# Kernel tuning notes

Hardware: AMD Instinct MI355X
Metric: run time of the kernel (lower is better)

## Reference

```python
import jax, jax.numpy as jnp
import numpy as np

N_SRC = 50000; N_DST = 50000; E = 800000
IN_NODE = 128; IN_EDGE = 16; OUT_NODE = 64; OUT_EDGE = 16; H = 4
LEAKY_SLOPE = 0.01  # F.leaky_relu default used inside dgl EGATConv


def setup_inputs() -> dict:
    key = jax.random.key(0)
    ks = jax.random.split(key, 11)
    return dict(
        nfeats=jax.random.normal(ks[0], (N_SRC, IN_NODE), jnp.float32),
        dst_feats=jax.random.normal(ks[1], (N_DST, IN_NODE), jnp.float32),
        reward=jax.random.uniform(ks[2], (E,), jnp.float32),
        src=jax.random.randint(ks[3], (E,), 0, N_SRC),
        dst=jax.random.randint(ks[4], (E,), 0, N_DST),
        W_ns=jax.random.normal(ks[5], (IN_NODE, H * OUT_NODE), jnp.float32) * 0.05,
        b_ns=jnp.zeros((H * OUT_NODE,), jnp.float32),
        W_ni=jax.random.normal(ks[6], (IN_NODE, H * OUT_EDGE), jnp.float32) * 0.05,
        W_nj=jax.random.normal(ks[7], (IN_NODE, H * OUT_EDGE), jnp.float32) * 0.05,
        W_fij=jax.random.normal(ks[8], (IN_EDGE, H * OUT_EDGE), jnp.float32) * 0.05,
        attn=jax.random.normal(ks[9], (H, OUT_EDGE), jnp.float32) * 0.05,
        b_e=jnp.zeros((H * OUT_EDGE,), jnp.float32),
    )


def reference(nfeats, dst_feats, reward, src, dst,
              W_ns, b_ns, W_ni, W_nj, W_fij, attn, b_e):
    # EGAT.forward with num_layers=1: efeats = reward repeated to IN_EDGE cols
    efeats = jnp.repeat(reward[:, None], IN_EDGE, axis=1)              # (E, Fe_in)
    # --- EGATConv ---
    f_ni = nfeats @ W_ni                                               # (Ns, H*Fe)
    f_nj = dst_feats @ W_nj                                            # (Nd, H*Fe)
    f_out = f_ni[src] + f_nj[dst] + efeats @ W_fij + b_e               # (E, H*Fe)
    f_out = jax.nn.leaky_relu(f_out, LEAKY_SLOPE).reshape(E, H, OUT_EDGE)
    e = jnp.einsum('ehf,hf->eh', f_out, attn)                          # (E, H)
    # edge softmax over incoming edges of each dst node (stable)
    m = jax.ops.segment_max(e, dst, num_segments=N_DST)                # (Nd, H)
    a = jnp.exp(e - m[dst])
    s = jax.ops.segment_sum(a, dst, num_segments=N_DST)                # (Nd, H)
    a = a / jnp.where(s > 0, s, 1.0)[dst]                              # (E, H)
    # weighted aggregation of projected src features
    h_src = (nfeats @ W_ns + b_ns).reshape(N_SRC, H, OUT_NODE)
    msg = h_src[src] * a[:, :, None]                                   # (E, H, Fn)
    h_out = jax.ops.segment_sum(msg, dst, num_segments=N_DST)          # (Nd, H, Fn)
    # wrapper: mean over heads then ReLU
    return jax.nn.relu(h_out.mean(axis=1))                             # (Nd, Fn)
```

## Files before the change

### kernel.cpp

```cpp
#include <hip/hip_runtime.h>

#define IN_NODE 128
#define OUT_NODE 64
#define NHEAD 4
#define HN 256
#define HE 64
#define LEAKY 0.01f

typedef __attribute__((ext_vector_type(8))) short bf16x8;
typedef __attribute__((ext_vector_type(4))) float f32x4;
typedef __attribute__((ext_vector_type(2))) float f32x2;

__device__ __forceinline__ float bf2f(unsigned short u) {
    union { unsigned u; float f; } v; v.u = ((unsigned)u) << 16; return v.f;
}
__device__ __forceinline__ unsigned short f2bf(float x) {
    union { float f; unsigned u; } v; v.f = x;
    unsigned r = v.u + 0x7FFF + ((v.u >> 16) & 1);
    return (unsigned short)(r >> 16);
}
__device__ __forceinline__ bf16x8 cvt8(float4 a, float4 b) {
    bf16x8 r;
    r[0] = (short)f2bf(a.x); r[1] = (short)f2bf(a.y);
    r[2] = (short)f2bf(a.z); r[3] = (short)f2bf(a.w);
    r[4] = (short)f2bf(b.x); r[5] = (short)f2bf(b.y);
    r[6] = (short)f2bf(b.z); r[7] = (short)f2bf(b.w);
    return r;
}
__device__ __forceinline__ f32x2 bfcvt2(unsigned d) {
    union { unsigned u; float f; } lo, hi;
    lo.u = d << 16; hi.u = d & 0xFFFF0000u;
    f32x2 r; r.x = lo.f; r.y = hi.f; return r;
}

__global__ void prep_hist(const float* __restrict__ W_fij,
                          const float* __restrict__ W_ni,
                          const float* __restrict__ W_ns,
                          const float* __restrict__ W_nj,
                          const int* __restrict__ dst,
                          float* __restrict__ wsum, unsigned short* __restrict__ WT,
                          int* __restrict__ cnt, int* __restrict__ rank, int E) {
    int b = blockIdx.x;
    if (b == 0) {
        int k = threadIdx.x;
        if (k < 64) {
            float s = 0.f;
#pragma unroll
            for (int c = 0; c < 16; ++c) s += W_fij[c * 64 + k];
            wsum[k] = s;
        }
        return;
    }
    if (b <= 12) {
        int base = (b - 1) * 4096 + threadIdx.x;
#pragma unroll
        for (int i = 0; i < 16; ++i) {
            int idx = base + i * 256;
            int g   = idx >> 11;
            int rem = idx & 2047;
            int c   = rem >> 9;
            int l   = (rem >> 3) & 63;
            int j   = rem & 7;
            int nl  = l & 15;
            int k   = c * 32 + (l >> 4) * 8 + j;
            unsigned short v;
            if (g < 4)       v = f2bf(W_ni[k * 64  + g * 16 + nl]);
            else if (g < 20) v = f2bf(W_ns[k * 256 + (g - 4) * 16 + nl]);
            else             v = f2bf(W_nj[k * 64  + (g - 20) * 16 + nl]);
            WT[idx] = v;
        }
        return;
    }
    int i = (b - 13) * 256 + threadIdx.x;
    if (i < E) rank[i] = atomicAdd(&cnt[dst[i]], 1);
}

__global__ __launch_bounds__(256) void scan_all(const int* __restrict__ cnt,
                                                int* __restrict__ row_ptr,
                                                int* __restrict__ partials,
                                                int* __restrict__ flags,
                                                int n, int E, int nb) {
    __shared__ int sums[256];
    __shared__ int s_base;
    int tid = threadIdx.x, b = blockIdx.x;
    int base = b * 1024;
    int v[4]; int tsum = 0;
#pragma unroll
    for (int j = 0; j < 4; ++j) {
        int idx = base + tid * 4 + j;
        v[j] = (idx < n) ? cnt[idx] : 0;
        tsum += v[j];
    }
    sums[tid] = tsum;
    __syncthreads();
    for (int off = 1; off < 256; off <<= 1) {
        int x = (tid >= off) ? sums[tid - off] : 0;
        __syncthreads();
        sums[tid] += x;
        __syncthreads();
    }
    if (tid == 255) {
        __hip_atomic_store(&partials[b], sums[255], __ATOMIC_RELAXED, __HIP_MEMORY_SCOPE_AGENT);
        __hip_atomic_store(&flags[b], 1, __ATOMIC_RELEASE, __HIP_MEMORY_SCOPE_AGENT);
    }
    if (tid < 64) {
        int val = 0;
        if (tid < nb) {
            while (__hip_atomic_load(&flags[tid], __ATOMIC_ACQUIRE, __HIP_MEMORY_SCOPE_AGENT) == 0) {
                __builtin_amdgcn_s_sleep(1);
            }
            val = __hip_atomic_load(&partials[tid], __ATOMIC_RELAXED, __HIP_MEMORY_SCOPE_AGENT);
        }
#pragma unroll
        for (int o = 1; o < 64; o <<= 1) {
            int x = __shfl_up(val, o);
            if (tid >= o) val += x;
        }
        int off = (b > 0) ? __shfl(val, b - 1) : 0;
        if (tid == 0) s_base = off;
    }
    __syncthreads();
    int run = s_base + sums[tid] - tsum;
#pragma unroll
    for (int j = 0; j < 4; ++j) {
        int idx = base + tid * 4 + j;
        if (idx < n) row_ptr[idx] = run;
        run += v[j];
    }
    if (b == nb - 1 && tid == 0) row_ptr[n] = E;
}

template<int NG, int G0>
__device__ __forceinline__ void gemm_tile(
    const float* __restrict__ A, int rowBase, int M,
    const unsigned short* __restrict__ WB, const float* __restrict__ b_ns,
    unsigned short* __restrict__ f_ni, unsigned short* __restrict__ h_src,
    unsigned short* __restrict__ f_nj, unsigned short* As)
{
    const int t = threadIdx.x;
    const float4* A4 = reinterpret_cast<const float4*>(A);
#pragma unroll
    for (int j = 0; j < 4; ++j) {
        int gi = j * 256 + t;
        int r  = gi >> 4;
        int gr = rowBase + r; if (gr >= M) gr = M - 1;
        int fi = (gi & 15) * 2;
        float4 a0 = A4[(size_t)gr * 32 + fi];
        float4 a1 = A4[(size_t)gr * 32 + fi + 1];
        int byteoff = (gi * 16) ^ ((r & 7) << 4);
        *reinterpret_cast<bf16x8*>(reinterpret_cast<char*>(As) + byteoff) = cvt8(a0, a1);
    }
    __syncthreads();

    const int lane = t & 63, w = t >> 6;
    const int rw = rowBase + w * 16;
    if (rw >= M) return;
    const int m = lane & 15, q = lane >> 4;
    const int tr = w * 16 + m;

    f32x4 acc[NG] = {};
    const char* Asb = reinterpret_cast<const char*>(As);
#pragma unroll
    for (int c = 0; c < 4; ++c) {
        int gi  = tr * 16 + c * 4 + q;
        int off = (gi * 16) ^ ((tr & 7) << 4);
        bf16x8 af = *reinterpret_cast<const bf16x8*>(Asb + off);
#pragma unroll
        for (int g = 0; g < NG; ++g) {
            bf16x8 bf = *reinterpret_cast<const bf16x8*>(
                WB + (size_t)(((G0 + g) * 4 + c) * 64 + lane) * 8);
            acc[g] = __builtin_amdgcn_mfma_f32_16x16x32_bf16(af, bf, acc[g], 0, 0, 0);
        }
    }

#pragma unroll
    for (int g = 0; g < NG; ++g) {
        const int ga = G0 + g;
        unsigned short* C; int N, colBase; const float* bias = nullptr;
        if (ga < 4)       { C = f_ni;  N = 64;  colBase = ga * 16; }
        else if (ga < 20) { C = h_src; N = 256; colBase = (ga - 4) * 16; bias = b_ns; }
        else              { C = f_nj;  N = 64;  colBase = (ga - 20) * 16; }
        int col = colBase + m;
        float bv = bias ? bias[col] : 0.f;
#pragma unroll
        for (int rr = 0; rr < 4; ++rr) {
            int orow = rw + q * 4 + rr;
            if (orow < M) C[(size_t)orow * N + col] = f2bf(acc[g][rr] + bv);
        }
    }
}

__global__ __launch_bounds__(256) void mega(
    const float* __restrict__ nfeats, const float* __restrict__ dst_feats,
    const unsigned short* __restrict__ WT, const float* __restrict__ b_ns,
    const int* __restrict__ src, const int* __restrict__ dst,
    const float* __restrict__ reward, const int* __restrict__ row_ptr,
    const int* __restrict__ rank,
    unsigned short* __restrict__ f_ni, unsigned short* __restrict__ h_src,
    unsigned short* __restrict__ f_nj, int2* __restrict__ sr_s,
    int Ns, int Nd, int E, int nBlkNf, int nBlkDj, int nScatter)
{
    __shared__ __align__(16) unsigned short As[64 * 128];
    const int g = blockIdx.x / 3, r = blockIdx.x % 3;
    if (r == 0) {
        if (g < 2 * nBlkNf) {
            int tile = g >> 1;
            if ((g & 1) == 0)
                gemm_tile<10, 0>(nfeats, tile * 64, Ns, WT, b_ns, f_ni, h_src, f_nj, As);
            else
                gemm_tile<10, 10>(nfeats, tile * 64, Ns, WT, b_ns, f_ni, h_src, f_nj, As);
        } else if (g < 2 * nBlkNf + nBlkDj) {
            gemm_tile<4, 20>(dst_feats, (g - 2 * nBlkNf) * 64, Nd, WT, b_ns, f_ni, h_src, f_nj, As);
        }
        return;
    }
    const int sb = g * 2 + (r - 1);
    if (sb >= nScatter) return;
    int i = sb * 256 + threadIdx.x;
    if (i >= E) return;
    int d = dst[i];
    int pos = row_ptr[d] + rank[i];
    sr_s[pos] = make_int2(src[i], __float_as_int(reward[i]));
}

struct G { uint2 ui; uint4 h0; uint4 h1; };
__device__ __forceinline__ G gatherE(const unsigned short* __restrict__ f_ni,
                                     const unsigned short* __restrict__ h_src,
                                     int sn, int ll, int hq) {
    G g;
    g.ui = *reinterpret_cast<const uint2*>(f_ni + (size_t)sn * HE + 4 * ll);
    const unsigned short* hp = h_src + (size_t)sn * HN + hq;
    g.h0 = *reinterpret_cast<const uint4*>(hp);
    g.h1 = *reinterpret_cast<const uint4*>(hp + 8);
    return g;
}

__global__ __launch_bounds__(256) void fused_agg(
    const unsigned short* __restrict__ f_ni, const unsigned short* __restrict__ f_nj,
    const unsigned short* __restrict__ h_src, const int2* __restrict__ sr_s,
    const int* __restrict__ row_ptr,
    const float* __restrict__ wsum, const float* __restrict__ b_e,
    const float* __restrict__ attn, float* __restrict__ out, int Nd)
{
    __shared__ float red[4][1024];
    const int wv = threadIdx.x >> 6, lane = threadIdx.x & 63;
    const int d = blockIdx.x * 4 + wv;
    if (d >= Nd) return;
    const int ll = lane & 15, sub = lane >> 4;
    const int hq = ((lane >> 2) & 3) * 64 + (lane & 3) * 16;
    const int mql = (lane >> 1) & 3;

    float4 wsv = *reinterpret_cast<const float4*>(wsum + 4 * ll);
    float4 bev = *reinterpret_cast<const float4*>(b_e + 4 * ll);
    float4 atv = *reinterpret_cast<const float4*>(attn + 4 * ll);
    f32x2 ws01 = {wsv.x, wsv.y}, ws23 = {wsv.z, wsv.w};
    f32x2 at01 = {atv.x, atv.y}, at23 = {atv.z, atv.w};
    const f32x2 lk2 = {LEAKY, LEAKY};

    const int beg = row_ptr[d];
    const int end = row_ptr[d + 1];
    const int deg = end - beg;

    float den = 0.f;
    f32x2 a0 = {}, a1 = {}, a2 = {}, a3 = {}, a4 = {}, a5 = {}, a6 = {}, a7 = {};

    if (deg > 0) {
        uint2 uj = *reinterpret_cast<const uint2*>(f_nj + (size_t)d * HE + 4 * ll);
        f32x2 bb01 = bfcvt2(uj.x) + (f32x2){bev.x, bev.y};
        f32x2 bb23 = bfcvt2(uj.y) + (f32x2){bev.z, bev.w};
        const int nq = (deg + 3) >> 2;
        const int last = end - 1;

#define LDSR(q) ({ int qq_ = ((q) < nq) ? (q) : (nq - 1);                 \
                   int slot_ = beg + qq_ * 4 + sub;                       \
                   if (slot_ > last) slot_ = last;                        \
                   sr_s[slot_]; })

#define COMPUTE(sr, gg, kq) do {                                          \
    float r_ = __int_as_float((sr).y);                                    \
    f32x2 r2_ = {r_, r_};                                                 \
    f32x2 v01_ = bfcvt2((gg).ui.x) + r2_ * ws01 + bb01;                   \
    f32x2 v23_ = bfcvt2((gg).ui.y) + r2_ * ws23 + bb23;                   \
    v01_ = __builtin_elementwise_max(v01_, v01_ * lk2);                   \
    v23_ = __builtin_elementwise_max(v23_, v23_ * lk2);                   \
    f32x2 t2_ = v01_ * at01 + v23_ * at23;                                \
    float t_ = t2_.x + t2_.y;                                             \
    t_ += __shfl_xor(t_, 1);                                              \
    t_ += __shfl_xor(t_, 2);                                              \
    float ev_ = ((beg + (kq) * 4 + sub) < end) ? __expf(t_) : 0.f;        \
    den += ev_;                                                           \
    f32x2 ev2_ = {ev_, ev_};                                              \
    a0 += bfcvt2((gg).h0.x) * ev2_;                                       \
    a1 += bfcvt2((gg).h0.y) * ev2_;                                       \
    a2 += bfcvt2((gg).h0.z) * ev2_;                                       \
    a3 += bfcvt2((gg).h0.w) * ev2_;                                       \
    a4 += bfcvt2((gg).h1.x) * ev2_;                                       \
    a5 += bfcvt2((gg).h1.y) * ev2_;                                       \
    a6 += bfcvt2((gg).h1.z) * ev2_;                                       \
    a7 += bfcvt2((gg).h1.w) * ev2_;                                       \
} while (0)

        int2 sr0 = LDSR(0), sr1 = LDSR(1);
        G gA = gatherE(f_ni, h_src, sr0.x, ll, hq);
        for (int k = 0; k < nq; ++k) {
            int2 sr2 = LDSR(k + 2);
            G gB = gatherE(f_ni, h_src, sr1.x, ll, hq);
            COMPUTE(sr0, gA, k);
            sr0 = sr1; sr1 = sr2; gA = gB;
        }
#undef COMPUTE
#undef LDSR
    }

    den += __shfl_xor(den, 16);
    den += __shfl_xor(den, 32);
    float sc = (den > 0.f) ? 0.25f / den : 0.f;
    float* wr = &red[wv][lane * 16];
    float4 s0 = {a0.x * sc, a0.y * sc, a1.x * sc, a1.y * sc};
    float4 s1 = {a2.x * sc, a2.y * sc, a3.x * sc, a3.y * sc};
    float4 s2 = {a4.x * sc, a4.y * sc, a5.x * sc, a5.y * sc};
    float4 s3 = {a6.x * sc, a6.y * sc, a7.x * sc, a7.y * sc};
    *reinterpret_cast<float4*>(wr + ((0 ^ mql) << 2)) = s0;
    *reinterpret_cast<float4*>(wr + ((1 ^ mql) << 2)) = s1;
    *reinterpret_cast<float4*>(wr + ((2 ^ mql) << 2)) = s2;
    *reinterpret_cast<float4*>(wr + ((3 ^ mql) << 2)) = s3;
    asm volatile("s_waitcnt lgkmcnt(0)" ::: "memory");
    float ssum = 0.f;
    const int e = lane & 15, c45 = lane >> 4;
#pragma unroll
    for (int s = 0; s < 4; ++s)
#pragma unroll
        for (int h = 0; h < 4; ++h) {
            int L = s * 16 + h * 4 + c45;
            int m2 = (L >> 1) & 3;
            int fi = L * 16 + (((e >> 2) ^ m2) << 2) + (e & 3);
            ssum += red[wv][fi];
        }
    out[(size_t)d * OUT_NODE + lane] = fmaxf(ssum, 0.f);
}

static inline char* align256(char* p) {
    return (char*)(((uintptr_t)p + 255) & ~(uintptr_t)255);
}

extern "C" void kernel_launch(void* const* d_in, const int* in_sizes, int n_in,
                              void* d_out, int out_size, void* d_ws, size_t ws_size,
                              hipStream_t stream) {
    const float* nfeats    = (const float*)d_in[0];
    const float* dst_feats = (const float*)d_in[1];
    const float* reward    = (const float*)d_in[2];
    const int*   src       = (const int*)d_in[3];
    const int*   dst       = (const int*)d_in[4];
    const float* W_ns      = (const float*)d_in[5];
    const float* b_ns      = (const float*)d_in[6];
    const float* W_ni      = (const float*)d_in[7];
    const float* W_nj      = (const float*)d_in[8];
    const float* W_fij     = (const float*)d_in[9];
    const float* attn      = (const float*)d_in[10];
    const float* b_e       = (const float*)d_in[11];
    float* out = (float*)d_out;

    const int Ns = in_sizes[0] / IN_NODE;
    const int Nd = in_sizes[1] / IN_NODE;
    const int E  = in_sizes[2];

    char* ws = (char*)d_ws;
    unsigned short* f_ni  = (unsigned short*)ws; ws = align256(ws + (size_t)Ns * HE * 2);
    unsigned short* f_nj  = (unsigned short*)ws; ws = align256(ws + (size_t)Nd * HE * 2);
    unsigned short* h_src = (unsigned short*)ws; ws = align256(ws + (size_t)Ns * HN * 2);
    unsigned short* WT    = (unsigned short*)ws; ws = align256(ws + 49152 * 2);
    float* wsum    = (float*)ws; ws = align256(ws + HE * 4);
    int*   cnt     = (int*)ws;
    int*   flags   = cnt + Nd;   ws = align256(ws + (size_t)(Nd + 64) * 4);
    int*   row_ptr = (int*)ws;   ws = align256(ws + (size_t)(Nd + 1) * 4);
    int*   partials= (int*)ws;   ws = align256(ws + 256 * 4);
    int2*  sr_s    = (int2*)ws;  ws = align256(ws + (size_t)E * 8);
    int*   rank    = (int*)ws;   ws = align256(ws + (size_t)E * 4);

    hipMemsetAsync(cnt, 0, (size_t)(Nd + 64) * 4, stream);

    prep_hist<<<13 + (E + 255) / 256, 256, 0, stream>>>(
        W_fij, W_ni, W_ns, W_nj, dst, wsum, WT, cnt, rank, E);

    int nb = (Nd + 1023) / 1024;
    scan_all<<<nb, 256, 0, stream>>>(cnt, row_ptr, partials, flags, Nd, E, nb);

    int nBlkNf = (Ns + 63) / 64;
    int nBlkDj = (Nd + 63) / 64;
    int nG = 2 * nBlkNf + nBlkDj;
    int nScatter = (E + 255) / 256;
    int nGroups = (nG > (nScatter + 1) / 2) ? nG : (nScatter + 1) / 2;
    mega<<<nGroups * 3, 256, 0, stream>>>(
        nfeats, dst_feats, WT, b_ns, src, dst, reward, row_ptr, rank,
        f_ni, h_src, f_nj, sr_s, Ns, Nd, E, nBlkNf, nBlkDj, nScatter);

    fused_agg<<<(Nd + 3) / 4, 256, 0, stream>>>(
        f_ni, f_nj, h_src, sr_s, row_ptr, wsum, b_e, attn, out, Nd);
}
```

Before: 256.9 us.

## Overlap degree histogram with projection GEMM and split scatter into own kernel

The per-edge atomic histogram of destination degrees moves out of the weight-prep kernel and is interleaved with the node-projection GEMM tiles in one launch. The CSR scatter, which needs the scan result, becomes a separate small kernel after the scan. The aim is to hide the atomic histogram behind GEMM work and shorten the serial prep kernel. The cost is one extra kernel launch, and the scatter no longer overlaps the GEMM as it did before.

Measured after the change: 259.6 us. About the same (+1.0%).

```diff
diff --git a/kernel.cpp b/kernel.cpp
--- a/kernel.cpp
+++ b/kernel.cpp
@@ -33,13 +33,11 @@
     f32x2 r; r.x = lo.f; r.y = hi.f; return r;
 }
 
-__global__ void prep_hist(const float* __restrict__ W_fij,
-                          const float* __restrict__ W_ni,
-                          const float* __restrict__ W_ns,
-                          const float* __restrict__ W_nj,
-                          const int* __restrict__ dst,
-                          float* __restrict__ wsum, unsigned short* __restrict__ WT,
-                          int* __restrict__ cnt, int* __restrict__ rank, int E) {
+__global__ void prep_w(const float* __restrict__ W_fij,
+                       const float* __restrict__ W_ni,
+                       const float* __restrict__ W_ns,
+                       const float* __restrict__ W_nj,
+                       float* __restrict__ wsum, unsigned short* __restrict__ WT) {
     int b = blockIdx.x;
     if (b == 0) {
         int k = threadIdx.x;
@@ -51,28 +49,23 @@
         }
         return;
     }
-    if (b <= 12) {
-        int base = (b - 1) * 4096 + threadIdx.x;
-#pragma unroll
-        for (int i = 0; i < 16; ++i) {
-            int idx = base + i * 256;
-            int g   = idx >> 11;
-            int rem = idx & 2047;
-            int c   = rem >> 9;
-            int l   = (rem >> 3) & 63;
-            int j   = rem & 7;
-            int nl  = l & 15;
-            int k   = c * 32 + (l >> 4) * 8 + j;
-            unsigned short v;
-            if (g < 4)       v = f2bf(W_ni[k * 64  + g * 16 + nl]);
-            else if (g < 20) v = f2bf(W_ns[k * 256 + (g - 4) * 16 + nl]);
-            else             v = f2bf(W_nj[k * 64  + (g - 20) * 16 + nl]);
-            WT[idx] = v;
-        }
-        return;
-    }
-    int i = (b - 13) * 256 + threadIdx.x;
-    if (i < E) rank[i] = atomicAdd(&cnt[dst[i]], 1);
+    int base = (b - 1) * 4096 + threadIdx.x;
+#pragma unroll
+    for (int i = 0; i < 16; ++i) {
+        int idx = base + i * 256;
+        int g   = idx >> 11;
+        int rem = idx & 2047;
+        int c   = rem >> 9;
+        int l   = (rem >> 3) & 63;
+        int j   = rem & 7;
+        int nl  = l & 15;
+        int k   = c * 32 + (l >> 4) * 8 + j;
+        unsigned short v;
+        if (g < 4)       v = f2bf(W_ni[k * 64  + g * 16 + nl]);
+        else if (g < 20) v = f2bf(W_ns[k * 256 + (g - 4) * 16 + nl]);
+        else             v = f2bf(W_nj[k * 64  + (g - 20) * 16 + nl]);
+        WT[idx] = v;
+    }
 }
 
 __global__ __launch_bounds__(256) void scan_all(const int* __restrict__ cnt,
@@ -190,19 +183,18 @@
     }
 }
 
-__global__ __launch_bounds__(256) void mega(
+__global__ __launch_bounds__(256) void hist_gemm(
     const float* __restrict__ nfeats, const float* __restrict__ dst_feats,
     const unsigned short* __restrict__ WT, const float* __restrict__ b_ns,
-    const int* __restrict__ src, const int* __restrict__ dst,
-    const float* __restrict__ reward, const int* __restrict__ row_ptr,
-    const int* __restrict__ rank,
+    const int* __restrict__ dst,
+    int* __restrict__ cnt, int* __restrict__ rank,
     unsigned short* __restrict__ f_ni, unsigned short* __restrict__ h_src,
-    unsigned short* __restrict__ f_nj, int2* __restrict__ sr_s,
-    int Ns, int Nd, int E, int nBlkNf, int nBlkDj, int nScatter)
+    unsigned short* __restrict__ f_nj,
+    int Ns, int Nd, int E, int nBlkNf, int nBlkDj)
 {
     __shared__ __align__(16) unsigned short As[64 * 128];
-    const int g = blockIdx.x / 3, r = blockIdx.x % 3;
-    if (r == 0) {
+    const int g = blockIdx.x >> 1, r = blockIdx.x & 1;
+    if (r == 1) {
         if (g < 2 * nBlkNf) {
             int tile = g >> 1;
             if ((g & 1) == 0)
@@ -214,13 +206,19 @@
         }
         return;
     }
-    const int sb = g * 2 + (r - 1);
-    if (sb >= nScatter) return;
-    int i = sb * 256 + threadIdx.x;
+    int i = g * 256 + threadIdx.x;
+    if (i < E) rank[i] = atomicAdd(&cnt[dst[i]], 1);
+}
+
+__global__ __launch_bounds__(256) void scatter_k(
+    const int* __restrict__ src, const int* __restrict__ dst,
+    const float* __restrict__ reward, const int* __restrict__ row_ptr,
+    const int* __restrict__ rank, int2* __restrict__ sr_s, int E)
+{
+    int i = blockIdx.x * 256 + threadIdx.x;
     if (i >= E) return;
     int d = dst[i];
-    int pos = row_ptr[d] + rank[i];
-    sr_s[pos] = make_int2(src[i], __float_as_int(reward[i]));
+    sr_s[row_ptr[d] + rank[i]] = make_int2(src[i], __float_as_int(reward[i]));
 }
 
 struct G { uint2 ui; uint4 h0; uint4 h1; };
@@ -379,20 +377,22 @@
 
     hipMemsetAsync(cnt, 0, (size_t)(Nd + 64) * 4, stream);
 
-    prep_hist<<<13 + (E + 255) / 256, 256, 0, stream>>>(
-        W_fij, W_ni, W_ns, W_nj, dst, wsum, WT, cnt, rank, E);
+    prep_w<<<13, 256, 0, stream>>>(W_fij, W_ni, W_ns, W_nj, wsum, WT);
+
+    int nBlkNf = (Ns + 63) / 64;
+    int nBlkDj = (Nd + 63) / 64;
+    int nU = 2 * nBlkNf + nBlkDj;
+    int nHist = (E + 255) / 256;
+    int nGroups = (nHist > nU) ? nHist : nU;
+    hist_gemm<<<nGroups * 2, 256, 0, stream>>>(
+        nfeats, dst_feats, WT, b_ns, dst, cnt, rank,
+        f_ni, h_src, f_nj, Ns, Nd, E, nBlkNf, nBlkDj);
 
     int nb = (Nd + 1023) / 1024;
     scan_all<<<nb, 256, 0, stream>>>(cnt, row_ptr, partials, flags, Nd, E, nb);
 
-    int nBlkNf = (Ns + 63) / 64;
-    int nBlkDj = (Nd + 63) / 64;
-    int nG = 2 * nBlkNf + nBlkDj;
-    int nScatter = (E + 255) / 256;
-    int nGroups = (nG > (nScatter + 1) / 2) ? nG : (nScatter + 1) / 2;
-    mega<<<nGroups * 3, 256, 0, stream>>>(
-        nfeats, dst_feats, WT, b_ns, src, dst, reward, row_ptr, rank,
-        f_ni, h_src, f_nj, sr_s, Ns, Nd, E, nBlkNf, nBlkDj, nScatter);
+    scatter_k<<<(E + 255) / 256, 256, 0, stream>>>(
+        src, dst, reward, row_ptr, rank, sr_s, E);
 
     fused_agg<<<(Nd + 3) / 4, 256, 0, stream>>>(
         f_ni, f_nj, h_src, sr_s, row_ptr, wsum, b_e, attn, out, Nd);
```
